# Optimization experiments

Measured on AMD Instinct MI355X. Metric: run time of the kernel, lower is better.

The kernel has to match this reference:

```python
import jax, jax.numpy as jnp
import numpy as np

B = 1                 # images
GRID = 30             # patch grid per side (HEIGHT_FACTOR*2)
NIMG = GRID * GRID    # 900 tokens per image
EMBED = 1152
HEADS = 16
DH = EMBED // HEADS   # 72
DHH = DH // 2         # 36
LAYERS = 6
FF = 4608             # mlp intermediate (4*EMBED)
MERGE = 2
MHID = EMBED * MERGE * MERGE   # 4608 merger hidden
OUT = 2048
DS_IDX = (2, 5)
PS = 16               # spatial patch size
TP = 2                # temporal patch size
THETA = 10000.0


def _rope_cos_sin():
    # 2D rotary positions in merge-block order: (Hf, Wf, mh, mw)
    HF = GRID // MERGE
    I, J, MH, MW = np.meshgrid(np.arange(HF), np.arange(HF), np.arange(MERGE), np.arange(MERGE), indexing='ij')
    hpos = (I * MERGE + MH).reshape(-1).astype(np.float32)
    wpos = (J * MERGE + MW).reshape(-1).astype(np.float32)
    inv = 1.0 / (THETA ** (np.arange(0, DHH, 2, dtype=np.float32) / DHH))      # [DH//4]
    rot = np.concatenate([hpos[:, None] * inv, wpos[:, None] * inv], axis=-1)  # [NIMG, DHH]
    cos = np.concatenate([np.cos(rot), np.cos(rot)], axis=-1)[None, None]      # [1,1,NIMG,DH]
    sin = np.concatenate([np.sin(rot), np.sin(rot)], axis=-1)[None, None]
    return jnp.asarray(cos, jnp.float32), jnp.asarray(sin, jnp.float32)


def _ln(x, w, b, eps=1e-6):
    mu = x.mean(-1, keepdims=True)
    xc = x - mu
    v = (xc * xc).mean(-1, keepdims=True)
    return xc * jax.lax.rsqrt(v + eps) * w + b


def _rot_half(t):
    t1, t2 = jnp.split(t, 2, axis=-1)
    return jnp.concatenate([-t2, t1], axis=-1)


def setup_inputs():
    key = jax.random.key(0)
    ks = jax.random.split(key, 12)
    s = 0.02
    n = lambda k, sh: jax.random.normal(k, sh, jnp.float32) * s
    z = lambda sh: jnp.zeros(sh, jnp.float32)
    o = lambda sh: jnp.ones(sh, jnp.float32)
    cos, sin = _rope_cos_sin()
    return {
        'pixel_values': jax.random.uniform(ks[0], (B, 1, 3, GRID * PS, GRID * PS), jnp.float32) * 255.0,
        'patch_w': n(ks[1], (EMBED, 3 * TP * PS * PS)), 'patch_b': z((EMBED,)),
        'pos_emb': n(ks[2], (1, NIMG, EMBED)),
        'cos': cos, 'sin': sin,
        'ln1_w': o((LAYERS, EMBED)), 'ln1_b': z((LAYERS, EMBED)),
        'qkv_w': n(ks[3], (LAYERS, 3 * EMBED, EMBED)), 'qkv_b': z((LAYERS, 3 * EMBED)),
        'proj_w': n(ks[4], (LAYERS, EMBED, EMBED)), 'proj_b': z((LAYERS, EMBED)),
        'ln2_w': o((LAYERS, EMBED)), 'ln2_b': z((LAYERS, EMBED)),
        'fc1_w': n(ks[5], (LAYERS, FF, EMBED)), 'fc1_b': z((LAYERS, FF)),
        'fc2_w': n(ks[6], (LAYERS, EMBED, FF)), 'fc2_b': z((LAYERS, EMBED)),
        'ds_norm_w': o((2, MHID)), 'ds_norm_b': z((2, MHID)),
        'ds_fc1_w': n(ks[7], (2, MHID, MHID)), 'ds_fc1_b': z((2, MHID)),
        'ds_fc2_w': n(ks[8], (2, OUT, MHID)), 'ds_fc2_b': z((2, OUT)),
        'm_norm_w': o((EMBED,)), 'm_norm_b': z((EMBED,)),
        'm_fc1_w': n(ks[9], (MHID, MHID)), 'm_fc1_b': z((MHID,)),
        'm_fc2_w': n(ks[10], (OUT, MHID)), 'm_fc2_b': z((OUT,)),
    }


def _forward(pixel_values, patch_w, patch_b, pos_emb, cos, sin, ln1_w, ln1_b, qkv_w, qkv_b, proj_w, proj_b, ln2_w, ln2_b, fc1_w, fc1_b, fc2_w, fc2_b, ds_norm_w, ds_norm_b, ds_fc1_w, ds_fc1_b, ds_fc2_w, ds_fc2_b, m_norm_w, m_norm_b, m_fc1_w, m_fc1_b, m_fc2_w, m_fc2_b):
    HF = GRID // MERGE
    x = (pixel_values - 127.5) * (1.0 / 127.5)                 # [B,1,3,H,W]
    x = jnp.concatenate([x, x], axis=1)                        # temporal duplication -> [B,2,3,H,W]
    x = x.reshape(B, 1, TP, 3, HF, MERGE, PS, HF, MERGE, PS)
    x = jnp.transpose(x, (0, 1, 4, 7, 5, 8, 3, 2, 6, 9))       # [B,1,HF,WF,mh,mw,3,TP,ps,ps]
    x = x.reshape(-1, 3 * TP * PS * PS)                        # [B*NIMG, 1536] (conv3d == matmul)
    h = (x @ patch_w.T + patch_b).reshape(1, -1, EMBED)        # [1, N, E]
    N = B * NIMG
    h = h + jnp.tile(pos_emb, (1, B, 1))
    cosf = jnp.tile(cos, (1, 1, B, 1))                         # [1,1,N,DH]
    sinf = jnp.tile(sin, (1, 1, B, 1))
    ds = []
    for l in range(LAYERS):
        hn = _ln(h, ln1_w[l], ln1_b[l])
        qkv = (hn @ qkv_w[l].T + qkv_b[l]).reshape(N, 3, HEADS, DH)
        qkv = jnp.transpose(qkv, (1, 2, 0, 3))                 # [3, H, N, dh]
        q, k, v = qkv[0][None], qkv[1][None], qkv[2][None]     # [1, H, N, dh]
        q = q * cosf + _rot_half(q) * sinf                     # inline RoPE (q,k pre-scaled by dh**-0.25 in weights)
        k = k * cosf + _rot_half(k) * sinf
        qb = jnp.transpose(q[0].reshape(HEADS, B, NIMG, DH), (1, 0, 2, 3))  # per-image attention blocks
        kb = jnp.transpose(k[0].reshape(HEADS, B, NIMG, DH), (1, 0, 2, 3))
        vb = jnp.transpose(v[0].reshape(HEADS, B, NIMG, DH), (1, 0, 2, 3))
        attn = jax.nn.softmax(jnp.einsum('bhqd,bhkd->bhqk', qb, kb), axis=-1)
        o = jnp.einsum('bhqk,bhkd->bhqd', attn, vb)            # [B, H, NIMG, dh]
        o = jnp.transpose(o, (0, 2, 1, 3)).reshape(1, N, EMBED)
        h = h + (o @ proj_w[l].T + proj_b[l])
        m = jax.nn.gelu(_ln(h, ln2_w[l], ln2_b[l]) @ fc1_w[l].T + fc1_b[l], approximate=True)
        h = h + (m @ fc2_w[l].T + fc2_b[l])
        if l in DS_IDX:
            d = DS_IDX.index(l)
            xm = _ln(h.reshape(1, -1, MHID), ds_norm_w[d], ds_norm_b[d])
            xm = jax.nn.gelu(xm @ ds_fc1_w[d].T + ds_fc1_b[d], approximate=True) @ ds_fc2_w[d].T + ds_fc2_b[d]
            ds.append(xm)                                      # [1, N/4, OUT]
    hm = _ln(h, m_norm_w, m_norm_b).reshape(1, -1, MHID)
    out = jax.nn.gelu(hm @ m_fc1_w.T + m_fc1_b, approximate=True) @ m_fc2_w.T + m_fc2_b
    return ds, out


def reference(pixel_values, patch_w, patch_b, pos_emb, cos, sin, ln1_w, ln1_b, qkv_w, qkv_b, proj_w, proj_b, ln2_w, ln2_b, fc1_w, fc1_b, fc2_w, fc2_b, ds_norm_w, ds_norm_b, ds_fc1_w, ds_fc1_b, ds_fc2_w, ds_fc2_b, m_norm_w, m_norm_b, m_fc1_w, m_fc1_b, m_fc2_w, m_fc2_b):
    ds, out = _forward(pixel_values, patch_w, patch_b, pos_emb, cos, sin, ln1_w, ln1_b, qkv_w, qkv_b, proj_w, proj_b, ln2_w, ln2_b, fc1_w, fc1_b, fc2_w, fc2_b, ds_norm_w, ds_norm_b, ds_fc1_w, ds_fc1_b, ds_fc2_w, ds_fc2_b, m_norm_w, m_norm_b, m_fc1_w, m_fc1_b, m_fc2_w, m_fc2_b)
    return (*ds, out)
```

## Files before the change

### kernel.cpp

```cpp
#include <hip/hip_runtime.h>
#include <hip/hip_bf16.h>
#include <cstdint>

#define NT   900
#define EMB  1152
#define NH   16
#define DHD  72
#define DHH  36
#define DHP  96
#define KVP  928
#define NL   6
#define FFD  4608
#define MHD  4608
#define OUTD 2048
#define NM   225

typedef __attribute__((ext_vector_type(8))) short short8;
typedef __attribute__((ext_vector_type(4))) float f32x4;

__device__ __forceinline__ ushort f2bf(float f) {
    uint32_t u = __float_as_uint(f);
    uint32_t r = u + 0x7FFF + ((u >> 16) & 1);
    return (ushort)(r >> 16);
}
__device__ __forceinline__ float gelu_f(float x) {
    return 0.5f * x * (1.0f + tanhf(0.7978845608f * (x + 0.044715f * x * x * x)));
}

__device__ __forceinline__ void g2lds16(const ushort* g, ushort* l) {
    __builtin_amdgcn_global_load_lds(
        (const __attribute__((address_space(1))) unsigned int*)g,
        (__attribute__((address_space(3))) unsigned int*)l, 16, 0, 0);
}

__global__ __launch_bounds__(256) void k_cvt(const float* __restrict__ src,
                                             ushort* __restrict__ dst, int n4) {
    int idx = blockIdx.x * 256 + threadIdx.x;
    if (idx >= n4) return;
    const float4 v = *(const float4*)(src + (size_t)idx * 4);
    ushort o[4] = { f2bf(v.x), f2bf(v.y), f2bf(v.z), f2bf(v.w) };
    *(uint2*)(dst + (size_t)idx * 4) = *(const uint2*)o;
}

__global__ __launch_bounds__(256) void k_patch(const float* __restrict__ pix,
                                               ushort* __restrict__ xp) {
    int idx = blockIdx.x * 256 + threadIdx.x;
    if (idx >= NT * 1536) return;
    int t = idx / 1536, f = idx - t * 1536;
    int mw = t & 1, mh = (t >> 1) & 1;
    int tq = t >> 2;
    int jj = tq % 15, ii = tq / 15;
    int pw = f & 15, ph = (f >> 4) & 15, c = f >> 9;
    int Hi = (ii * 2 + mh) * 16 + ph;
    int Wi = (jj * 2 + mw) * 16 + pw;
    float p = pix[((size_t)c * 480 + Hi) * 480 + Wi];
    xp[idx] = f2bf((p - 127.5f) * (1.0f / 127.5f));
}

__global__ __launch_bounds__(256) void k_ln(const float* __restrict__ x,
                                            const float* __restrict__ w,
                                            const float* __restrict__ b,
                                            ushort* __restrict__ y, int C) {
    int row = blockIdx.x;
    int tid = threadIdx.x;
    const float* xr = x + (size_t)row * C;
    float s = 0.f, ss = 0.f;
    for (int c = tid; c < C; c += 256) { float v = xr[c]; s += v; ss += v * v; }
    for (int off = 32; off; off >>= 1) {
        s  += __shfl_down(s,  off, 64);
        ss += __shfl_down(ss, off, 64);
    }
    __shared__ float rs[4], rss[4];
    int wid = tid >> 6, lane = tid & 63;
    if (lane == 0) { rs[wid] = s; rss[wid] = ss; }
    __syncthreads();
    float S  = rs[0] + rs[1] + rs[2] + rs[3];
    float SS = rss[0] + rss[1] + rss[2] + rss[3];
    float mu  = S / C;
    float var = SS / C - mu * mu;
    float inv = rsqrtf(var + 1e-6f);
    ushort* yr = y + (size_t)row * C;
    for (int c = tid; c < C; c += 256) yr[c] = f2bf((xr[c] - mu) * inv * w[c] + b[c]);
}

template <int ACT, int OBF16, int SPLIT>
__global__ __launch_bounds__(256) void k_bgs(const ushort* __restrict__ A,
                                             const ushort* __restrict__ W,
                                             const float* __restrict__ bias,
                                             const float* __restrict__ res,
                                             void* __restrict__ Cp,
                                             float* __restrict__ part,
                                             int M, int N, int K, int S) {
    __shared__ __align__(16) ushort As[64 * 64];
    __shared__ __align__(16) ushort Bs[64 * 64];
    int tid = threadIdx.x;
    int row0 = blockIdx.x * 64, col0 = blockIdx.y * 64;
    int z = blockIdx.z;
    int Kc = K / S;
    int kbeg = z * Kc;
    int steps = Kc >> 6;

    int w = tid >> 6, lane = tid & 63;
    int lrow = lane >> 3;
    int cg   = ((lane & 7) ^ lrow) << 3;

    int ar0 = row0 + w * 16 + lrow; if (ar0 > M - 1) ar0 = M - 1;
    int ar1 = row0 + w * 16 + 8 + lrow; if (ar1 > M - 1) ar1 = M - 1;
    int wr0 = col0 + w * 16 + lrow;
    int wr1 = wr0 + 8;
    const ushort* ap0 = A + (size_t)ar0 * K + kbeg + cg;
    const ushort* ap1 = A + (size_t)ar1 * K + kbeg + cg;
    const ushort* wp0 = W + (size_t)wr0 * K + kbeg + cg;
    const ushort* wp1 = W + (size_t)wr1 * K + kbeg + cg;
    ushort* asd0 = &As[(w * 16) * 64];
    ushort* asd1 = &As[(w * 16 + 8) * 64];
    ushort* bsd0 = &Bs[(w * 16) * 64];
    ushort* bsd1 = &Bs[(w * 16 + 8) * 64];

    int fr = lane & 15, kg8 = (lane >> 4) << 3;
    int wrr = (w >> 1) * 32, wcc = (w & 1) * 32;
    int sw = (fr & 7) << 3;

    f32x4 acc[2][2] = {};
    for (int s = 0; s < steps; ++s) {
        int kk = s << 6;
        __syncthreads();
        g2lds16(ap0 + kk, asd0);
        g2lds16(ap1 + kk, asd1);
        g2lds16(wp0 + kk, bsd0);
        g2lds16(wp1 + kk, bsd1);
        __syncthreads();
#pragma unroll
        for (int j = 0; j < 2; ++j) {
            int ko = j * 32 + kg8;
            int kx = ko ^ sw;
            short8 a0 = *(const short8*)&As[(wrr + fr) * 64 + kx];
            short8 a1 = *(const short8*)&As[(wrr + 16 + fr) * 64 + kx];
            short8 b0 = *(const short8*)&Bs[(wcc + fr) * 64 + kx];
            short8 b1 = *(const short8*)&Bs[(wcc + 16 + fr) * 64 + kx];
            acc[0][0] = __builtin_amdgcn_mfma_f32_16x16x32_bf16(a0, b0, acc[0][0], 0, 0, 0);
            acc[0][1] = __builtin_amdgcn_mfma_f32_16x16x32_bf16(a0, b1, acc[0][1], 0, 0, 0);
            acc[1][0] = __builtin_amdgcn_mfma_f32_16x16x32_bf16(a1, b0, acc[1][0], 0, 0, 0);
            acc[1][1] = __builtin_amdgcn_mfma_f32_16x16x32_bf16(a1, b1, acc[1][1], 0, 0, 0);
        }
    }

#pragma unroll
    for (int fi = 0; fi < 2; fi++)
#pragma unroll
        for (int fj = 0; fj < 2; fj++)
#pragma unroll
            for (int r = 0; r < 4; r++) {
                int row = row0 + wrr + fi * 16 + (lane >> 4) * 4 + r;
                int col = col0 + wcc + fj * 16 + fr;
                if (row < M) {
                    if (SPLIT) {
                        part[((size_t)z * M + row) * N + col] = acc[fi][fj][r];
                    } else {
                        float v = acc[fi][fj][r] + bias[col];
                        if (res) v += res[(size_t)row * N + col];
                        if (ACT == 1) v = gelu_f(v);
                        if (OBF16) ((ushort*)Cp)[(size_t)row * N + col] = f2bf(v);
                        else       ((float*)Cp)[(size_t)row * N + col] = v;
                    }
                }
            }
}

template <int ACT, int OBF16>
__global__ __launch_bounds__(256) void k_fix(const float* __restrict__ part,
                                             const float* __restrict__ bias,
                                             const float* __restrict__ res,
                                             void* __restrict__ Cp,
                                             int M, int N, int S) {
    size_t idx = (size_t)blockIdx.x * 256 + threadIdx.x;
    size_t total = (size_t)M * N / 4;
    if (idx >= total) return;
    size_t e = idx * 4;
    int row = (int)(e / N), col = (int)(e - (size_t)row * N);
    float4 v = *(const float4*)(part + e);
    for (int s = 1; s < S; ++s) {
        const float4 p = *(const float4*)(part + (size_t)s * M * N + e);
        v.x += p.x; v.y += p.y; v.z += p.z; v.w += p.w;
    }
    const float4 bi = *(const float4*)(bias + col);
    v.x += bi.x; v.y += bi.y; v.z += bi.z; v.w += bi.w;
    if (res) {
        const float4 rr = *(const float4*)(res + e);
        v.x += rr.x; v.y += rr.y; v.z += rr.z; v.w += rr.w;
    }
    if (ACT == 1) { v.x = gelu_f(v.x); v.y = gelu_f(v.y); v.z = gelu_f(v.z); v.w = gelu_f(v.w); }
    if (OBF16) {
        ushort o[4] = { f2bf(v.x), f2bf(v.y), f2bf(v.z), f2bf(v.w) };
        *(uint2*)((ushort*)Cp + e) = *(const uint2*)o;
    } else {
        *(float4*)((float*)Cp + e) = v;
    }
}

template <int OBF16>
__global__ __launch_bounds__(256) void k_mm(const ushort* __restrict__ A,
                                            const ushort* __restrict__ Wb,
                                            void* __restrict__ Cp,
                                            int M, int N, int K, int ldc, int Nw,
                                            long as_, long ws_, long cs_) {
    __shared__ __align__(16) ushort As[64 * 40];
    __shared__ __align__(16) ushort Bs[64 * 40];
    int z = blockIdx.z;
    A  += (size_t)z * as_;
    Wb += (size_t)z * ws_;
    float*  Cf = (float*)Cp + (size_t)z * cs_;
    ushort* Cb = (ushort*)Cp + (size_t)z * cs_;

    int tid = threadIdx.x;
    int row0 = blockIdx.y * 64, col0 = blockIdx.x * 64;

    int sm = tid >> 2, sp = tid & 3;
    int ar = row0 + sm; if (ar > M - 1) ar = M - 1;
    int wr = col0 + sm; if (wr > N - 1) wr = N - 1;
    const ushort* aptr = A + (size_t)ar * K;

    int lane = tid & 63, wid = tid >> 6;
    int wrr = (wid >> 1) * 32, wcc = (wid & 1) * 32;
    int fr = lane & 15, kg = lane >> 4;

    f32x4 acc[2][2] = {};

    for (int k0 = 0; k0 < K; k0 += 32) {
        *(uint4*)&As[sm * 40 + sp * 8] = *(const uint4*)(aptr + k0 + sp * 8);
        *(uint4*)&Bs[sm * 40 + sp * 8] = *(const uint4*)(Wb + (size_t)wr * K + k0 + sp * 8);
        __syncthreads();
        short8 a0 = *(const short8*)&As[(wrr + fr) * 40 + kg * 8];
        short8 a1 = *(const short8*)&As[(wrr + 16 + fr) * 40 + kg * 8];
        short8 b0 = *(const short8*)&Bs[(wcc + fr) * 40 + kg * 8];
        short8 b1 = *(const short8*)&Bs[(wcc + 16 + fr) * 40 + kg * 8];
        acc[0][0] = __builtin_amdgcn_mfma_f32_16x16x32_bf16(a0, b0, acc[0][0], 0, 0, 0);
        acc[0][1] = __builtin_amdgcn_mfma_f32_16x16x32_bf16(a0, b1, acc[0][1], 0, 0, 0);
        acc[1][0] = __builtin_amdgcn_mfma_f32_16x16x32_bf16(a1, b0, acc[1][0], 0, 0, 0);
        acc[1][1] = __builtin_amdgcn_mfma_f32_16x16x32_bf16(a1, b1, acc[1][1], 0, 0, 0);
        __syncthreads();
    }

#pragma unroll
    for (int fi = 0; fi < 2; fi++)
#pragma unroll
        for (int fj = 0; fj < 2; fj++)
#pragma unroll
            for (int r = 0; r < 4; r++) {
                int row = row0 + wrr + fi * 16 + (lane >> 4) * 4 + r;
                int col = col0 + wcc + fj * 16 + (lane & 15);
                if (row < M && col < Nw) {
                    float v = acc[fi][fj][r];
                    if (OBF16) Cb[(size_t)row * ldc + col] = f2bf(v);
                    else       Cf[(size_t)row * ldc + col] = v;
                }
            }
}

__global__ __launch_bounds__(256) void k_rope(const float* __restrict__ qkv,
                                              const float* __restrict__ cs,
                                              const float* __restrict__ sn,
                                              ushort* __restrict__ q,
                                              ushort* __restrict__ k,
                                              ushort* __restrict__ vt) {
    int idx = blockIdx.x * 256 + threadIdx.x;
    if (idx >= NT * NH * DHP) return;
    int t = idx / (NH * DHP);
    int rem = idx - t * (NH * DHP);
    int h = rem / DHP, d = rem - h * DHP;
    size_t oi = ((size_t)h * NT + t) * DHP + d;
    if (d < DHD) {
        const float* base = qkv + (size_t)t * 3 * EMB;
        float c = cs[t * DHD + d], s = sn[t * DHD + d];
        int   d2 = (d < DHH) ? d + DHH : d - DHH;
        float sg = (d < DHH) ? -1.f : 1.f;
        int e = h * DHD + d;
        float qv = base[e] * c + sg * base[h * DHD + d2] * s;
        float kv = base[EMB + e] * c + sg * base[EMB + h * DHD + d2] * s;
        q[oi] = f2bf(qv);
        k[oi] = f2bf(kv);
        vt[((size_t)h * DHP + d) * KVP + t] = f2bf(base[2 * EMB + e]);
    } else {
        q[oi] = 0;
        k[oi] = 0;
    }
}

__global__ __launch_bounds__(256) void k_vpad(ushort* __restrict__ vt) {
    int idx = blockIdx.x * 256 + threadIdx.x;
    int tot = NH * DHP * (KVP - NT);
    if (idx >= tot) return;
    int pw = KVP - NT;
    int hd = idx / pw, j = idx - hd * pw;
    vt[(size_t)hd * KVP + NT + j] = 0;
}

__global__ __launch_bounds__(256) void k_sm(const float* __restrict__ S,
                                            ushort* __restrict__ P) {
    int row = blockIdx.x * 4 + (threadIdx.x >> 6);
    int lane = threadIdx.x & 63;
    const float* sp = S + (size_t)row * KVP;
    ushort* pp = P + (size_t)row * KVP;
    float v[15];
#pragma unroll
    for (int i = 0; i < 15; i++) {
        int kt = lane + i * 64;
        v[i] = (kt < NT) ? sp[kt] : -1e30f;
    }
    float mx = -1e30f;
#pragma unroll
    for (int i = 0; i < 15; i++) mx = fmaxf(mx, v[i]);
    for (int off = 32; off; off >>= 1) mx = fmaxf(mx, __shfl_xor(mx, off, 64));
    float sum = 0.f;
#pragma unroll
    for (int i = 0; i < 15; i++) {
        int kt = lane + i * 64;
        v[i] = (kt < NT) ? __expf(v[i] - mx) : 0.f;
        sum += v[i];
    }
    for (int off = 32; off; off >>= 1) sum += __shfl_xor(sum, off, 64);
    float inv = 1.f / sum;
#pragma unroll
    for (int i = 0; i < 15; i++) {
        int kt = lane + i * 64;
        if (kt < KVP) pp[kt] = f2bf(v[i] * inv);
    }
}

extern "C" void kernel_launch(void* const* d_in, const int* in_sizes, int n_in,
                              void* d_out, int out_size, void* d_ws, size_t ws_size,
                              hipStream_t stream) {
    const float* pix     = (const float*)d_in[0];
    const float* patch_w = (const float*)d_in[1];
    const float* patch_b = (const float*)d_in[2];
    const float* pos_emb = (const float*)d_in[3];
    const float* cosb    = (const float*)d_in[4];
    const float* sinb    = (const float*)d_in[5];
    const float* ln1_w   = (const float*)d_in[6];
    const float* ln1_b   = (const float*)d_in[7];
    const float* qkv_w   = (const float*)d_in[8];
    const float* qkv_b   = (const float*)d_in[9];
    const float* proj_w  = (const float*)d_in[10];
    const float* proj_b  = (const float*)d_in[11];
    const float* ln2_w   = (const float*)d_in[12];
    const float* ln2_b   = (const float*)d_in[13];
    const float* fc1_w   = (const float*)d_in[14];
    const float* fc1_b   = (const float*)d_in[15];
    const float* fc2_w   = (const float*)d_in[16];
    const float* fc2_b   = (const float*)d_in[17];
    const float* dsn_w   = (const float*)d_in[18];
    const float* dsn_b   = (const float*)d_in[19];
    const float* ds1_w   = (const float*)d_in[20];
    const float* ds1_b   = (const float*)d_in[21];
    const float* ds2_w   = (const float*)d_in[22];
    const float* ds2_b   = (const float*)d_in[23];
    const float* mn_w    = (const float*)d_in[24];
    const float* mn_b    = (const float*)d_in[25];
    const float* mf1_w   = (const float*)d_in[26];
    const float* mf1_b   = (const float*)d_in[27];
    const float* mf2_w   = (const float*)d_in[28];
    const float* mf2_b   = (const float*)d_in[29];
    float* out = (float*)d_out;

    float* wsf = (float*)d_ws;
    size_t off = 0;
    auto af = [&](size_t n) { float* p = wsf + off; off += (n + 3) & ~(size_t)3; return p; };
    float* h    = af((size_t)NT * EMB);
    float* qkv  = af((size_t)NT * 3 * EMB);
    float* part = af((size_t)4 * NT * EMB);
    float* S    = af((size_t)NH * NT * KVP);
    ushort* wsh = (ushort*)(wsf + off);
    size_t hoff = 0;
    auto ah = [&](size_t n) { ushort* p = wsh + hoff; hoff += (n + 7) & ~(size_t)7; return p; };
    ushort* hn  = ah((size_t)NT * EMB);
    ushort* qb  = ah((size_t)NH * NT * DHP);
    ushort* kb  = ah((size_t)NH * NT * DHP);
    ushort* vt  = ah((size_t)NH * DHP * KVP);
    ushort* P   = ah((size_t)NH * NT * KVP);
    ushort* ob  = ah((size_t)NT * EMB);
    ushort* t1  = ah((size_t)NT * FFD);
    ushort* xp  = t1;
    ushort* w_patch = ah((size_t)EMB * 1536);
    ushort* w_qkv   = ah((size_t)NL * 3 * EMB * EMB);
    ushort* w_proj  = ah((size_t)NL * EMB * EMB);
    ushort* w_fc1   = ah((size_t)NL * FFD * EMB);
    ushort* w_fc2   = ah((size_t)NL * EMB * FFD);
    ushort* w_ds1   = ah((size_t)2 * MHD * MHD);
    ushort* w_ds2   = ah((size_t)2 * OUTD * MHD);
    ushort* w_mf1   = ah((size_t)MHD * MHD);
    ushort* w_mf2   = ah((size_t)OUTD * MHD);

    const long QS = (long)NT * DHP;
    const long VS = (long)DHP * KVP;
    const long SS = (long)NT * KVP;

    const int MB  = (NT + 63) / 64;
    const int MBm = (NM + 63) / 64;
    auto fixg = [](int M, int N) { return dim3(((size_t)M * N / 4 + 255) / 256); };
    auto cvt = [&](const float* s, ushort* d, size_t n) {
        k_cvt<<<dim3((unsigned)((n / 4 + 255) / 256)), 256, 0, stream>>>(s, d, (int)(n / 4));
    };

    cvt(patch_w, w_patch, (size_t)EMB * 1536);
    cvt(qkv_w,   w_qkv,   (size_t)NL * 3 * EMB * EMB);
    cvt(proj_w,  w_proj,  (size_t)NL * EMB * EMB);
    cvt(fc1_w,   w_fc1,   (size_t)NL * FFD * EMB);
    cvt(fc2_w,   w_fc2,   (size_t)NL * EMB * FFD);
    cvt(ds1_w,   w_ds1,   (size_t)2 * MHD * MHD);
    cvt(ds2_w,   w_ds2,   (size_t)2 * OUTD * MHD);
    cvt(mf1_w,   w_mf1,   (size_t)MHD * MHD);
    cvt(mf2_w,   w_mf2,   (size_t)OUTD * MHD);

    k_patch<<<dim3((NT * 1536 + 255) / 256), 256, 0, stream>>>(pix, xp);
    k_vpad<<<dim3((NH * DHP * (KVP - NT) + 255) / 256), 256, 0, stream>>>(vt);
    k_bgs<0, 0, 1><<<dim3(MB, EMB / 64, 2), 256, 0, stream>>>(
        xp, w_patch, nullptr, nullptr, nullptr, part, NT, EMB, 1536, 2);
    k_fix<0, 0><<<fixg(NT, EMB), 256, 0, stream>>>(part, patch_b, pos_emb, h, NT, EMB, 2);

    for (int l = 0; l < NL; ++l) {
        k_ln<<<NT, 256, 0, stream>>>(h, ln1_w + l * EMB, ln1_b + l * EMB, hn, EMB);
        k_bgs<0, 0, 0><<<dim3(MB, 3 * EMB / 64, 1), 256, 0, stream>>>(
            hn, w_qkv + (size_t)l * 3 * EMB * EMB, qkv_b + l * 3 * EMB, nullptr, qkv,
            nullptr, NT, 3 * EMB, EMB, 1);
        k_rope<<<dim3((NT * NH * DHP + 255) / 256), 256, 0, stream>>>(
            qkv, cosb, sinb, qb, kb, vt);
        k_mm<0><<<dim3(MB, MB, NH), 256, 0, stream>>>(
            qb, kb, S, NT, NT, DHP, KVP, NT, QS, QS, SS);
        k_sm<<<dim3(NH * NT / 4), 256, 0, stream>>>(S, P);
        k_mm<1><<<dim3(2, MB, NH), 256, 0, stream>>>(
            P, vt, ob, NT, DHD, KVP, EMB, DHD, SS, VS, DHD);
        k_bgs<0, 0, 1><<<dim3(MB, EMB / 64, 3), 256, 0, stream>>>(
            ob, w_proj + (size_t)l * EMB * EMB, nullptr, nullptr, nullptr, part,
            NT, EMB, EMB, 3);
        k_fix<0, 0><<<fixg(NT, EMB), 256, 0, stream>>>(part, proj_b + l * EMB, h, h,
                                                       NT, EMB, 3);
        k_ln<<<NT, 256, 0, stream>>>(h, ln2_w + l * EMB, ln2_b + l * EMB, hn, EMB);
        k_bgs<1, 1, 0><<<dim3(MB, FFD / 64, 1), 256, 0, stream>>>(
            hn, w_fc1 + (size_t)l * FFD * EMB, fc1_b + l * FFD, nullptr, t1,
            nullptr, NT, FFD, EMB, 1);
        k_bgs<0, 0, 1><<<dim3(MB, EMB / 64, 4), 256, 0, stream>>>(
            t1, w_fc2 + (size_t)l * EMB * FFD, nullptr, nullptr, nullptr, part,
            NT, EMB, FFD, 4);
        k_fix<0, 0><<<fixg(NT, EMB), 256, 0, stream>>>(part, fc2_b + l * EMB, h, h,
                                                       NT, EMB, 4);
        if (l == 2 || l == 5) {
            int d = (l == 2) ? 0 : 1;
            k_ln<<<NM, 256, 0, stream>>>(h, dsn_w + d * MHD, dsn_b + d * MHD, hn, MHD);
            k_bgs<0, 0, 1><<<dim3(MBm, MHD / 64, 4), 256, 0, stream>>>(
                hn, w_ds1 + (size_t)d * MHD * MHD, nullptr, nullptr, nullptr, part,
                NM, MHD, MHD, 4);
            k_fix<1, 1><<<fixg(NM, MHD), 256, 0, stream>>>(part, ds1_b + d * MHD,
                                                           nullptr, t1, NM, MHD, 4);
            k_bgs<0, 0, 1><<<dim3(MBm, OUTD / 64, 4), 256, 0, stream>>>(
                t1, w_ds2 + (size_t)d * OUTD * MHD, nullptr, nullptr, nullptr, part,
                NM, OUTD, MHD, 4);
            k_fix<0, 0><<<fixg(NM, OUTD), 256, 0, stream>>>(
                part, ds2_b + d * OUTD, nullptr, out + (size_t)d * NM * OUTD,
                NM, OUTD, 4);
        }
    }
    k_ln<<<NT, 256, 0, stream>>>(h, mn_w, mn_b, hn, EMB);
    k_bgs<0, 0, 1><<<dim3(MBm, MHD / 64, 4), 256, 0, stream>>>(
        hn, w_mf1, nullptr, nullptr, nullptr, part, NM, MHD, MHD, 4);
    k_fix<1, 1><<<fixg(NM, MHD), 256, 0, stream>>>(part, mf1_b, nullptr, t1, NM, MHD, 4);
    k_bgs<0, 0, 1><<<dim3(MBm, OUTD / 64, 4), 256, 0, stream>>>(
        t1, w_mf2, nullptr, nullptr, nullptr, part, NM, OUTD, MHD, 4);
    k_fix<0, 0><<<fixg(NM, OUTD), 256, 0, stream>>>(
        part, mf2_b, nullptr, out + (size_t)2 * NM * OUTD, NM, OUTD, 4);
}
```

Baseline: 1.484 ms.

## Double-buffer LDS tiles in main GEMM and register-prefetch the batched GEMM

The main bf16 GEMM kernel gets two LDS buffers per operand. The next K-tile is loaded with g2lds16 while MFMAs run on the current one, which cuts the loop from two barriers per step to one. The batched attention GEMM now prefetches the next K-slice from global memory into registers before computing on the current LDS tile. The goal is to hide global-load latency behind MFMA work. The cost is double the LDS use in the main GEMM, which may lower occupancy. Correctness also now relies on the barrier ordering the asynchronous LDS writes correctly.

```diff
diff --git a/kernel.cpp b/kernel.cpp
--- a/kernel.cpp
+++ b/kernel.cpp
@@ -91,8 +91,8 @@
                                              void* __restrict__ Cp,
                                              float* __restrict__ part,
                                              int M, int N, int K, int S) {
-    __shared__ __align__(16) ushort As[64 * 64];
-    __shared__ __align__(16) ushort Bs[64 * 64];
+    __shared__ __align__(16) ushort As[2][64 * 64];
+    __shared__ __align__(16) ushort Bs[2][64 * 64];
     int tid = threadIdx.x;
     int row0 = blockIdx.x * 64, col0 = blockIdx.y * 64;
     int z = blockIdx.z;
@@ -112,37 +112,45 @@
     const ushort* ap1 = A + (size_t)ar1 * K + kbeg + cg;
     const ushort* wp0 = W + (size_t)wr0 * K + kbeg + cg;
     const ushort* wp1 = W + (size_t)wr1 * K + kbeg + cg;
-    ushort* asd0 = &As[(w * 16) * 64];
-    ushort* asd1 = &As[(w * 16 + 8) * 64];
-    ushort* bsd0 = &Bs[(w * 16) * 64];
-    ushort* bsd1 = &Bs[(w * 16 + 8) * 64];
+    int ld0 = (w * 16) * 64;
+    int ld1 = (w * 16 + 8) * 64;
 
     int fr = lane & 15, kg8 = (lane >> 4) << 3;
     int wrr = (w >> 1) * 32, wcc = (w & 1) * 32;
     int sw = (fr & 7) << 3;
 
     f32x4 acc[2][2] = {};
+    g2lds16(ap0, &As[0][ld0]);
+    g2lds16(ap1, &As[0][ld1]);
+    g2lds16(wp0, &Bs[0][ld0]);
+    g2lds16(wp1, &Bs[0][ld1]);
+    __syncthreads();
+
+    int cur = 0;
     for (int s = 0; s < steps; ++s) {
-        int kk = s << 6;
-        __syncthreads();
-        g2lds16(ap0 + kk, asd0);
-        g2lds16(ap1 + kk, asd1);
-        g2lds16(wp0 + kk, bsd0);
-        g2lds16(wp1 + kk, bsd1);
-        __syncthreads();
+        if (s + 1 < steps) {
+            int kk = (s + 1) << 6;
+            int nb = cur ^ 1;
+            g2lds16(ap0 + kk, &As[nb][ld0]);
+            g2lds16(ap1 + kk, &As[nb][ld1]);
+            g2lds16(wp0 + kk, &Bs[nb][ld0]);
+            g2lds16(wp1 + kk, &Bs[nb][ld1]);
+        }
 #pragma unroll
         for (int j = 0; j < 2; ++j) {
             int ko = j * 32 + kg8;
             int kx = ko ^ sw;
-            short8 a0 = *(const short8*)&As[(wrr + fr) * 64 + kx];
-            short8 a1 = *(const short8*)&As[(wrr + 16 + fr) * 64 + kx];
-            short8 b0 = *(const short8*)&Bs[(wcc + fr) * 64 + kx];
-            short8 b1 = *(const short8*)&Bs[(wcc + 16 + fr) * 64 + kx];
+            short8 a0 = *(const short8*)&As[cur][(wrr + fr) * 64 + kx];
+            short8 a1 = *(const short8*)&As[cur][(wrr + 16 + fr) * 64 + kx];
+            short8 b0 = *(const short8*)&Bs[cur][(wcc + fr) * 64 + kx];
+            short8 b1 = *(const short8*)&Bs[cur][(wcc + 16 + fr) * 64 + kx];
             acc[0][0] = __builtin_amdgcn_mfma_f32_16x16x32_bf16(a0, b0, acc[0][0], 0, 0, 0);
             acc[0][1] = __builtin_amdgcn_mfma_f32_16x16x32_bf16(a0, b1, acc[0][1], 0, 0, 0);
             acc[1][0] = __builtin_amdgcn_mfma_f32_16x16x32_bf16(a1, b0, acc[1][0], 0, 0, 0);
             acc[1][1] = __builtin_amdgcn_mfma_f32_16x16x32_bf16(a1, b1, acc[1][1], 0, 0, 0);
         }
+        __syncthreads();
+        cur ^= 1;
     }
 
 #pragma unroll
@@ -218,17 +226,27 @@
     int sm = tid >> 2, sp = tid & 3;
     int ar = row0 + sm; if (ar > M - 1) ar = M - 1;
     int wr = col0 + sm; if (wr > N - 1) wr = N - 1;
-    const ushort* aptr = A + (size_t)ar * K;
+    const ushort* aptr = A + (size_t)ar * K + sp * 8;
+    const ushort* wptr = Wb + (size_t)wr * K + sp * 8;
+    ushort* asd = &As[sm * 40 + sp * 8];
+    ushort* bsd = &Bs[sm * 40 + sp * 8];
 
     int lane = tid & 63, wid = tid >> 6;
     int wrr = (wid >> 1) * 32, wcc = (wid & 1) * 32;
     int fr = lane & 15, kg = lane >> 4;
 
     f32x4 acc[2][2] = {};
+    uint4 ra = *(const uint4*)aptr;
+    uint4 rb = *(const uint4*)wptr;
 
     for (int k0 = 0; k0 < K; k0 += 32) {
-        *(uint4*)&As[sm * 40 + sp * 8] = *(const uint4*)(aptr + k0 + sp * 8);
-        *(uint4*)&Bs[sm * 40 + sp * 8] = *(const uint4*)(Wb + (size_t)wr * K + k0 + sp * 8);
+        __syncthreads();
+        *(uint4*)asd = ra;
+        *(uint4*)bsd = rb;
+        if (k0 + 32 < K) {
+            ra = *(const uint4*)(aptr + k0 + 32);
+            rb = *(const uint4*)(wptr + k0 + 32);
+        }
         __syncthreads();
         short8 a0 = *(const short8*)&As[(wrr + fr) * 40 + kg * 8];
         short8 a1 = *(const short8*)&As[(wrr + 16 + fr) * 40 + kg * 8];
@@ -238,7 +256,6 @@
         acc[0][1] = __builtin_amdgcn_mfma_f32_16x16x32_bf16(a0, b1, acc[0][1], 0, 0, 0);
         acc[1][0] = __builtin_amdgcn_mfma_f32_16x16x32_bf16(a1, b0, acc[1][0], 0, 0, 0);
         acc[1][1] = __builtin_amdgcn_mfma_f32_16x16x32_bf16(a1, b1, acc[1][1], 0, 0, 0);
-        __syncthreads();
     }
 
 #pragma unroll
```

New measurement: 1.627 ms. +9.6%, slower.
